# Kernel tuning notes

Hardware: AMD Instinct MI355X
Metric: run time of the kernel (lower is better)

Reference implementation:

```python
import jax, jax.numpy as jnp
import numpy as np

LR = 1.0
THRESHOLD = 0.5
EPS = 1e-8


def _hebbian_mask(x, H):
    # x: [B, x_size], H: [y_size, x_size]
    xn = x / jnp.linalg.norm(x, axis=1, keepdims=True)
    y = xn @ H.T                                   # [B, y_size]
    yn = y / jnp.linalg.norm(y, axis=1, keepdims=True)
    theta = jnp.mean(yn ** 2)                      # scalar
    # sum over batch of outer products == GEMM: [y_size, x_size]
    H_new = H + LR * (jnp.einsum('by,bx->yx', yn, xn) - theta * H)
    score = jnp.sum(H_new, axis=1)                 # [y_size]
    score = (score - jnp.min(score)) / (jnp.max(score) - jnp.min(score) + EPS)
    return jnp.where(score < THRESHOLD, 0.0, 1.0).astype(x.dtype)


def setup_inputs() -> dict:
    key = jax.random.key(0)
    ks = jax.random.split(key, 12)
    B, D_IN, D_OUT = 8192, 1024, 1000
    h = [256, 128, 64]
    inp = {
        'x': jax.random.normal(ks[0], (B, D_IN), dtype=jnp.float32),
        'mask0': jnp.ones((h[0],), dtype=jnp.float32),
        'mask1': jnp.ones((h[1],), dtype=jnp.float32),
        'mask2': jnp.ones((h[2],), dtype=jnp.float32),
        # linear layer params (torch Linear: y = x @ W.T + b)
        'W1': jax.random.normal(ks[1], (h[0], D_IN), dtype=jnp.float32) * 0.02,
        'b1': jnp.zeros((h[0],), dtype=jnp.float32),
        'W2': jax.random.normal(ks[2], (h[1], h[0]), dtype=jnp.float32) * 0.02,
        'b2': jnp.zeros((h[1],), dtype=jnp.float32),
        'W3': jax.random.normal(ks[3], (h[2], h[1]), dtype=jnp.float32) * 0.02,
        'b3': jnp.zeros((h[2],), dtype=jnp.float32),
        'W4': jax.random.normal(ks[4], (D_OUT, h[2]), dtype=jnp.float32) * 0.02,
        'b4': jnp.zeros((D_OUT,), dtype=jnp.float32),
        # hebbian params, init N(0, 0.01) as in the module (4th never used in forward)
        'H1': jax.random.normal(ks[5], (h[0], D_IN), dtype=jnp.float32) * 0.01,
        'H2': jax.random.normal(ks[6], (h[1], h[0]), dtype=jnp.float32) * 0.01,
        'H3': jax.random.normal(ks[7], (h[2], h[1]), dtype=jnp.float32) * 0.01,
    }
    return inp


def reference(x, mask0, mask1, mask2, W1, b1, W2, b2, W3, b3, W4, b4, H1, H2, H3):
    # layer 1 (hebbian uses the layer *input*)
    hm0 = _hebbian_mask(x, H1)
    x1 = jax.nn.relu(x @ W1.T + b1) * mask0
    # layer 2
    hm1 = _hebbian_mask(x1, H2)
    x2 = jax.nn.relu(x1 @ W2.T + b2) * mask1
    # layer 3
    hm2 = _hebbian_mask(x2, H3)
    x3 = jax.nn.relu(x2 @ W3.T + b3) * mask2
    # layer 4 (relu applied, no mask, no hebbian)
    out = jax.nn.relu(x3 @ W4.T + b4)
    return (out, hm0, hm1, hm2)
```

## Files before the change

kernel.cpp:

```cpp
#include <hip/hip_runtime.h>
#include <math.h>

typedef __attribute__((ext_vector_type(8))) short short8;
typedef __attribute__((ext_vector_type(4))) float floatx4;

typedef __attribute__((address_space(1))) const unsigned int as1_uint;
typedef __attribute__((address_space(3))) unsigned int as3_uint;
#define GLD16(g, l) __builtin_amdgcn_global_load_lds((as1_uint*)(g), (as3_uint*)(l), 16, 0, 0)

__device__ __forceinline__ unsigned short f2bf(float f) {
    unsigned int u = __float_as_uint(f);
    return (unsigned short)((u + 0x7fffu + ((u >> 16) & 1u)) >> 16);
}
__device__ __forceinline__ float bf2f(unsigned short h) {
    return __uint_as_float(((unsigned int)h) << 16);
}

__global__ __launch_bounds__(256) void convert_x(
    const float* __restrict__ x, unsigned short* __restrict__ Axhl,
    float* __restrict__ rs1, float* __restrict__ rq1,
    float* __restrict__ rs2, float* __restrict__ rq2,
    float* __restrict__ rs3, float* __restrict__ rq3,
    float* __restrict__ score, int* __restrict__ ctr)
{
    const int row = blockIdx.x, tid = threadIdx.x;
    if (row == 0) { score[tid] = 0.f; if (tid < 8) ctr[tid] = 0; }
    if (tid == 0) { rs2[row] = 0.f; rq2[row] = 0.f; rs3[row] = 0.f; rq3[row] = 0.f; }
    float4 v = *(const float4*)(x + (size_t)row * 1024 + (tid << 2));
    ushort4 h, l;
    h.x = f2bf(v.x); l.x = f2bf(v.x - bf2f(h.x));
    h.y = f2bf(v.y); l.y = f2bf(v.y - bf2f(h.y));
    h.z = f2bf(v.z); l.z = f2bf(v.z - bf2f(h.z));
    h.w = f2bf(v.w); l.w = f2bf(v.w - bf2f(h.w));
    *(ushort4*)(Axhl + (size_t)row * 2048 + (tid << 2)) = h;
    *(ushort4*)(Axhl + (size_t)row * 2048 + 1024 + (tid << 2)) = l;
    float s = v.x + v.y + v.z + v.w;
    float qq = v.x*v.x + v.y*v.y + v.z*v.z + v.w*v.w;
#pragma unroll
    for (int d = 1; d < 64; d <<= 1) { s += __shfl_xor(s, d, 64); qq += __shfl_xor(qq, d, 64); }
    __shared__ float sS[4], sQ[4];
    if ((tid & 63) == 0) { sS[tid >> 6] = s; sQ[tid >> 6] = qq; }
    __syncthreads();
    if (tid == 0) {
        rs1[row] = sS[0] + sS[1] + sS[2] + sS[3];
        rq1[row] = sQ[0] + sQ[1] + sQ[2] + sQ[3];
    }
}

__global__ __launch_bounds__(256) void convert_w(
    const float* __restrict__ H1, const float* __restrict__ W1,
    const float* __restrict__ H2, const float* __restrict__ W2,
    const float* __restrict__ H3, const float* __restrict__ W3,
    const float* __restrict__ W4,
    unsigned short* __restrict__ B1, unsigned short* __restrict__ B2,
    unsigned short* __restrict__ B3, unsigned short* __restrict__ B4,
    float* __restrict__ rsH1, float* __restrict__ rsH2, float* __restrict__ rsH3)
{
    const int b = blockIdx.x, tid = threadIdx.x;
    const float* src; unsigned short* dst; int K; float* rsum = nullptr;
    if (b < 256)      { K = 1024; src = H1 + (size_t)b * 1024;        dst = B1 + (size_t)b * 2048;        rsum = rsH1 + b; }
    else if (b < 512) { K = 1024; src = W1 + (size_t)(b - 256) * 1024; dst = B1 + (size_t)b * 2048; }
    else if (b < 640) { K = 256;  src = H2 + (size_t)(b - 512) * 256;  dst = B2 + (size_t)(b - 512) * 512; rsum = rsH2 + (b - 512); }
    else if (b < 768) { K = 256;  src = W2 + (size_t)(b - 640) * 256;  dst = B2 + (size_t)(b - 512) * 512; }
    else if (b < 832) { K = 128;  src = H3 + (size_t)(b - 768) * 128;  dst = B3 + (size_t)(b - 768) * 256; rsum = rsH3 + (b - 768); }
    else if (b < 896) { K = 128;  src = W3 + (size_t)(b - 832) * 128;  dst = B3 + (size_t)(b - 768) * 256; }
    else { K = 64; int r = b - 896; src = (r < 1000) ? (W4 + (size_t)r * 64) : nullptr; dst = B4 + (size_t)r * 128; }

    float lsum = 0.f;
    if (tid * 4 < K) {
        float4 v = src ? *(const float4*)(src + tid * 4) : make_float4(0.f, 0.f, 0.f, 0.f);
        ushort4 h, l;
        h.x = f2bf(v.x); l.x = f2bf(v.x - bf2f(h.x));
        h.y = f2bf(v.y); l.y = f2bf(v.y - bf2f(h.y));
        h.z = f2bf(v.z); l.z = f2bf(v.z - bf2f(h.z));
        h.w = f2bf(v.w); l.w = f2bf(v.w - bf2f(h.w));
        *(ushort4*)(dst + tid * 4) = h;
        *(ushort4*)(dst + K + tid * 4) = l;
        lsum = v.x + v.y + v.z + v.w;
    }
    if (rsum) {
#pragma unroll
        for (int d = 1; d < 64; d <<= 1) lsum += __shfl_xor(lsum, d, 64);
        __shared__ float sS[4];
        if ((tid & 63) == 0) sS[tid >> 6] = lsum;
        __syncthreads();
        if (tid == 0) *rsum = sS[0] + sS[1] + sS[2] + sS[3];
    }
}

#define KW 64
__global__ __launch_bounds__(256) void mfma_layer(
    const unsigned short* __restrict__ Ag, const unsigned short* __restrict__ Bg,
    const float* __restrict__ bias, const float* __restrict__ maskv,
    float* __restrict__ T, unsigned short* __restrict__ Xhl,
    float* __restrict__ outF,
    float* __restrict__ rs, float* __restrict__ rq,
    int K, int Nh, int Nw, int NwReal)
{
    constexpr int CPR = 8;
    constexpr int PERW = 4;
    constexpr int TILEB = 128 * 128;
    __shared__ __align__(16) char lds[4 * TILEB];

    const int tid = threadIdx.x;
    const int w = tid >> 6, lane = tid & 63;
    const int q = lane >> 4, m16 = lane & 15;
    const int wm = w & 1, wn = w >> 1;

    const int lin = blockIdx.y * gridDim.x + blockIdx.x;
    const int g = lin & 7, s = lin >> 3;
    const int by = g + ((s & 7) << 3);
    const int bx = s >> 3;

    const int strideB = 4 * K;
    const int u = lane & 7, v = lane >> 3;
    int aOff[PERW], bOff[PERW];
#pragma unroll
    for (int t0 = 0; t0 < PERW; ++t0) {
        const int t = w * PERW + t0;
        const int r = t * 8 + v;
        const int c = u ^ (r & 7);
        aOff[t0] = (by * 128 + r) * strideB + c * 16;
        bOff[t0] = (bx * 128 + r) * strideB + c * 16;
    }

    const char* Ab = (const char*)Ag;
    const char* Bb = (const char*)Bg;
    floatx4 acc[4][4] = {};

    const int kiters = K / KW;
    const int NIT = 3 * kiters;

    auto stage = [&](int buf, int it) {
        const int seg = it / kiters;
        const int k0 = (it - seg * kiters) * KW;
        const int ka = ((seg == 1) ? 2 * K : 0) + 2 * k0;
        const int kb = ((seg == 2) ? 2 * K : 0) + 2 * k0;
        char* base = lds + buf * 2 * TILEB;
#pragma unroll
        for (int t0 = 0; t0 < PERW; ++t0) {
            const int t = w * PERW + t0;
            GLD16(Ab + aOff[t0] + ka, base + t * 1024);
            GLD16(Bb + bOff[t0] + kb, base + TILEB + t * 1024);
        }
    };

    stage(0, 0);
    int cur = 0;
    for (int it = 0; it < NIT; ++it) {
        __syncthreads();
        if (it + 1 < NIT) stage(cur ^ 1, it + 1);
        const char* pb = lds + cur * 2 * TILEB;
#pragma unroll
        for (int h = 0; h < 2; ++h) {
            short8 af[4], bfr[4];
#pragma unroll
            for (int i = 0; i < 4; ++i) {
                const int ra = wm * 64 + i * 16 + m16;
                af[i] = *(const short8*)(pb + ra * 128 + (((h * 4 + q) ^ (ra & 7)) << 4));
                const int rb = wn * 64 + i * 16 + m16;
                bfr[i] = *(const short8*)(pb + TILEB + rb * 128 + (((h * 4 + q) ^ (rb & 7)) << 4));
            }
#pragma unroll
            for (int i = 0; i < 4; ++i)
#pragma unroll
                for (int j = 0; j < 4; ++j)
                    acc[i][j] = __builtin_amdgcn_mfma_f32_16x16x32_bf16(af[i], bfr[j], acc[i][j], 0, 0, 0);
        }
        cur ^= 1;
    }

    const int colW = bx * 128 + wn * 64;
    const bool isHwave = (outF == nullptr) && (colW < Nh);
#pragma unroll
    for (int i = 0; i < 4; ++i) {
        const int row0 = by * 128 + wm * 64 + i * 16 + q * 4;
        float rsum[4] = {0.f, 0.f, 0.f, 0.f}, rqsum[4] = {0.f, 0.f, 0.f, 0.f};
#pragma unroll
        for (int j = 0; j < 4; ++j) {
            const int col = colW + j * 16 + m16;
            floatx4 vv = acc[i][j];
            if (outF) {
                if (col < NwReal) {
                    const float bb = bias[col];
#pragma unroll
                    for (int rg = 0; rg < 4; ++rg)
                        outF[(size_t)(row0 + rg) * NwReal + col] = fmaxf(vv[rg] + bb, 0.f);
                }
            } else if (isHwave) {
#pragma unroll
                for (int rg = 0; rg < 4; ++rg)
                    T[(size_t)(row0 + rg) * Nh + col] = vv[rg];
            } else {
                const int c = col - Nh;
                const float bb = bias[c], mm = maskv[c];
#pragma unroll
                for (int rg = 0; rg < 4; ++rg) {
                    const float xv = fmaxf(vv[rg] + bb, 0.f) * mm;
                    const unsigned short hi = f2bf(xv);
                    const unsigned short lo = f2bf(xv - bf2f(hi));
                    Xhl[(size_t)(row0 + rg) * (2 * Nw) + c] = hi;
                    Xhl[(size_t)(row0 + rg) * (2 * Nw) + Nw + c] = lo;
                    rsum[rg] += xv; rqsum[rg] += xv * xv;
                }
            }
        }
        if (rs && !isHwave && !outF) {
#pragma unroll
            for (int rg = 0; rg < 4; ++rg) {
                float a_ = rsum[rg], b_ = rqsum[rg];
#pragma unroll
                for (int d = 1; d < 16; d <<= 1) {
                    a_ += __shfl_xor(a_, d, 64);
                    b_ += __shfl_xor(b_, d, 64);
                }
                if (m16 == 0) {
                    atomicAdd(&rs[row0 + rg], a_);
                    atomicAdd(&rq[row0 + rg], b_);
                }
            }
        }
    }
}

__global__ __launch_bounds__(256) void hebb_finish(
    const float* __restrict__ T, const float* __restrict__ rs,
    const float* __restrict__ rq, const float* __restrict__ rowsumH,
    float* __restrict__ score, int* __restrict__ counter,
    float* __restrict__ hm, int ysize)
{
    const int tid = threadIdx.x, lane = tid & 63, wave = tid >> 6;
    const int vecsz = ysize >> 6;
    const int b0 = blockIdx.x * 64;
    float accv[4] = {0.f, 0.f, 0.f, 0.f};
    for (int r = wave; r < 64; r += 4) {
        const float* Trow = T + (size_t)(b0 + r) * ysize;
        float vals[4] = {0.f, 0.f, 0.f, 0.f};
        if (vecsz == 4) { float4 t = *(const float4*)(Trow + (lane << 2)); vals[0]=t.x; vals[1]=t.y; vals[2]=t.z; vals[3]=t.w; }
        else if (vecsz == 2) { float2 t = *(const float2*)(Trow + (lane << 1)); vals[0]=t.x; vals[1]=t.y; }
        else vals[0] = Trow[lane];
        float sq = vals[0]*vals[0] + vals[1]*vals[1] + vals[2]*vals[2] + vals[3]*vals[3];
#pragma unroll
        for (int i = 1; i < 64; i <<= 1) sq += __shfl_xor(sq, i, 64);
        const float wgt = rs[b0 + r] / (sqrtf(rq[b0 + r]) * sqrtf(sq));
        for (int j = 0; j < 4; ++j) accv[j] += vals[j] * wgt;
    }
    __shared__ float sPart[4][256];
    for (int j = 0; j < vecsz; ++j) sPart[wave][lane * vecsz + j] = accv[j];
    __syncthreads();
    if (tid < ysize)
        atomicAdd(&score[tid], sPart[0][tid] + sPart[1][tid] + sPart[2][tid] + sPart[3][tid]);
    __syncthreads();
    __shared__ int lastFlag;
    if (tid == 0) {
        __threadfence();
        lastFlag = (atomicAdd(counter, 1) == (int)gridDim.x - 1) ? 1 : 0;
    }
    __syncthreads();
    if (!lastFlag) return;
    float full = 0.f;
    if (tid < ysize) {
        float sc = atomicAdd(&score[tid], 0.f);
        full = (1.f - 1.f / (float)ysize) * rowsumH[tid] + sc;
    }
    __shared__ float sMin[256], sMax[256];
    sMin[tid] = (tid < ysize) ? full : 3.4e38f;
    sMax[tid] = (tid < ysize) ? full : -3.4e38f;
    __syncthreads();
    for (int st = 128; st > 0; st >>= 1) {
        if (tid < st) { sMin[tid] = fminf(sMin[tid], sMin[tid+st]); sMax[tid] = fmaxf(sMax[tid], sMax[tid+st]); }
        __syncthreads();
    }
    if (tid < ysize) {
        float nrm = (full - sMin[0]) / (sMax[0] - sMin[0] + 1e-8f);
        hm[tid] = (nrm < 0.5f) ? 0.f : 1.f;
    }
    score[tid] = 0.f;
}

extern "C" void kernel_launch(void* const* d_in, const int* in_sizes, int n_in,
                              void* d_out, int out_size, void* d_ws, size_t ws_size,
                              hipStream_t stream)
{
    const float* x     = (const float*)d_in[0];
    const float* mask0 = (const float*)d_in[1];
    const float* mask1 = (const float*)d_in[2];
    const float* mask2 = (const float*)d_in[3];
    const float* W1 = (const float*)d_in[4];  const float* b1 = (const float*)d_in[5];
    const float* W2 = (const float*)d_in[6];  const float* b2 = (const float*)d_in[7];
    const float* W3 = (const float*)d_in[8];  const float* b3 = (const float*)d_in[9];
    const float* W4 = (const float*)d_in[10]; const float* b4 = (const float*)d_in[11];
    const float* H1 = (const float*)d_in[12];
    const float* H2 = (const float*)d_in[13];
    const float* H3 = (const float*)d_in[14];

    float* out = (float*)d_out;
    float* hm0 = out + (size_t)8192 * 1000;
    float* hm1 = hm0 + 256;
    float* hm2 = hm1 + 128;

    float* ws = (float*)d_ws;
    unsigned short* Axhl = (unsigned short*)ws;
    unsigned short* X2hl = (unsigned short*)ws;
    unsigned short* X3hl = (unsigned short*)(ws + 1048576);
    float* p = ws + 8388608;
    unsigned short* B1 = (unsigned short*)p;  p += 524288;
    unsigned short* B2 = (unsigned short*)p;  p += 65536;
    unsigned short* B3 = (unsigned short*)p;  p += 16384;
    unsigned short* B4 = (unsigned short*)p;  p += 65536;
    float* T    = p;  p += 2097152;
    unsigned short* X1hl = (unsigned short*)p; p += 2097152;
    float* rs1 = p; p += 8192;  float* rq1 = p; p += 8192;
    float* rs2 = p; p += 8192;  float* rq2 = p; p += 8192;
    float* rs3 = p; p += 8192;  float* rq3 = p; p += 8192;
    float* rsH1 = p; p += 256;  float* rsH2 = p; p += 128;  float* rsH3 = p; p += 64;
    float* score = p; p += 256;
    int* ctr = (int*)p;

    convert_x<<<8192, 256, 0, stream>>>(x, Axhl, rs1, rq1, rs2, rq2, rs3, rq3, score, ctr);
    convert_w<<<1920, 256, 0, stream>>>(H1, W1, H2, W2, H3, W3, W4, B1, B2, B3, B4, rsH1, rsH2, rsH3);

    mfma_layer<<<dim3(4, 64), 256, 0, stream>>>(
        Axhl, B1, b1, mask0, T, X1hl, nullptr, rs2, rq2, 1024, 256, 256, 256);
    hebb_finish<<<128, 256, 0, stream>>>(T, rs1, rq1, rsH1, score, ctr + 0, hm0, 256);

    mfma_layer<<<dim3(2, 64), 256, 0, stream>>>(
        X1hl, B2, b2, mask1, T, X2hl, nullptr, rs3, rq3, 256, 128, 128, 128);
    hebb_finish<<<128, 256, 0, stream>>>(T, rs2, rq2, rsH2, score, ctr + 1, hm1, 128);

    mfma_layer<<<dim3(1, 64), 256, 0, stream>>>(
        X2hl, B3, b3, mask2, T, X3hl, nullptr, nullptr, nullptr, 128, 64, 64, 64);
    hebb_finish<<<128, 256, 0, stream>>>(T, rs3, rq3, rsH3, score, ctr + 2, hm2, 64);

    mfma_layer<<<dim3(8, 64), 256, 0, stream>>>(
        X3hl, B4, b4, nullptr, nullptr, nullptr, out, nullptr, nullptr, 64, 0, 1024, 1000);
}
```

Baseline: 243.5 us.

## Template MFMA layer on tile size and fuse split-bf16 passes per k-step

The GEMM kernel is templated on the M/N tile (128x64 or 64x64), so layers with small N launch more blocks and fill more CUs. The hi/lo bf16 split products (hh, lh, hl) are now computed together within each 32-wide k-step instead of in three sequential passes over K. Both the hi and lo parts of A and B are staged into LDS per step. The block-to-tile mapping is generalized for any grid height. Smaller tiles lower per-block data reuse and raise global traffic relative to compute.

```diff
diff --git a/kernel.cpp b/kernel.cpp
--- a/kernel.cpp
+++ b/kernel.cpp
@@ -88,7 +88,7 @@
     }
 }
 
-#define KW 64
+template<int TM, int TN>
 __global__ __launch_bounds__(256) void mfma_layer(
     const unsigned short* __restrict__ Ag, const unsigned short* __restrict__ Bg,
     const float* __restrict__ bias, const float* __restrict__ maskv,
@@ -97,10 +97,14 @@
     float* __restrict__ rs, float* __restrict__ rq,
     int K, int Nh, int Nw, int NwReal)
 {
-    constexpr int CPR = 8;
-    constexpr int PERW = 4;
-    constexpr int TILEB = 128 * 128;
-    __shared__ __align__(16) char lds[4 * TILEB];
+    constexpr int MI = TM / 32;
+    constexpr int NJ = TN / 32;
+    constexpr int IA = TM / 16;
+    constexpr int IB = TN / 16;
+    constexpr int NI = 2 * (IA + IB);
+    constexpr int PERW = NI / 4;
+    constexpr int BUFB = NI * 1024;
+    __shared__ __align__(16) char lds[2 * BUFB];
 
     const int tid = threadIdx.x;
     const int w = tid >> 6, lane = tid & 63;
@@ -108,76 +112,77 @@
     const int wm = w & 1, wn = w >> 1;
 
     const int lin = blockIdx.y * gridDim.x + blockIdx.x;
-    const int g = lin & 7, s = lin >> 3;
-    const int by = g + ((s & 7) << 3);
-    const int bx = s >> 3;
+    const int g = lin & 7, idx = lin >> 3;
+    const int rows8 = gridDim.y >> 3;
+    const int by = g + 8 * (idx % rows8);
+    const int bx = idx / rows8;
 
     const int strideB = 4 * K;
-    const int u = lane & 7, v = lane >> 3;
-    int aOff[PERW], bOff[PERW];
+    const int v = lane >> 2, u = lane & 3;
+
+    const char* srcp[PERW];
 #pragma unroll
     for (int t0 = 0; t0 < PERW; ++t0) {
         const int t = w * PERW + t0;
-        const int r = t * 8 + v;
-        const int c = u ^ (r & 7);
-        aOff[t0] = (by * 128 + r) * strideB + c * 16;
-        bOff[t0] = (bx * 128 + r) * strideB + c * 16;
-    }
-
-    const char* Ab = (const char*)Ag;
-    const char* Bb = (const char*)Bg;
-    floatx4 acc[4][4] = {};
-
-    const int kiters = K / KW;
-    const int NIT = 3 * kiters;
-
-    auto stage = [&](int buf, int it) {
-        const int seg = it / kiters;
-        const int k0 = (it - seg * kiters) * KW;
-        const int ka = ((seg == 1) ? 2 * K : 0) + 2 * k0;
-        const int kb = ((seg == 2) ? 2 * K : 0) + 2 * k0;
-        char* base = lds + buf * 2 * TILEB;
-#pragma unroll
-        for (int t0 = 0; t0 < PERW; ++t0) {
-            const int t = w * PERW + t0;
-            GLD16(Ab + aOff[t0] + ka, base + t * 1024);
-            GLD16(Bb + bOff[t0] + kb, base + TILEB + t * 1024);
-        }
+        int rloc; const char* base;
+        if (t < IA)               { rloc = t * 16 + v;                base = (const char*)Ag + (size_t)(by * TM + rloc) * strideB; }
+        else if (t < 2 * IA)      { rloc = (t - IA) * 16 + v;         base = (const char*)Ag + (size_t)(by * TM + rloc) * strideB + 2 * K; }
+        else if (t < 2 * IA + IB) { rloc = (t - 2 * IA) * 16 + v;     base = (const char*)Bg + (size_t)(bx * TN + rloc) * strideB; }
+        else                      { rloc = (t - 2 * IA - IB) * 16 + v; base = (const char*)Bg + (size_t)(bx * TN + rloc) * strideB + 2 * K; }
+        srcp[t0] = base + ((u ^ (rloc & 3)) << 4);
+    }
+
+    auto stage = [&](int buf, int k0) {
+        char* dst = lds + buf * BUFB + (w * PERW) * 1024;
+        const int kb = 2 * k0;
+#pragma unroll
+        for (int t0 = 0; t0 < PERW; ++t0)
+            GLD16(srcp[t0] + kb, dst + t0 * 1024);
     };
+
+    floatx4 acc[MI][NJ] = {};
+    const int NIT = K / 32;
 
     stage(0, 0);
     int cur = 0;
     for (int it = 0; it < NIT; ++it) {
         __syncthreads();
-        if (it + 1 < NIT) stage(cur ^ 1, it + 1);
-        const char* pb = lds + cur * 2 * TILEB;
-#pragma unroll
-        for (int h = 0; h < 2; ++h) {
-            short8 af[4], bfr[4];
-#pragma unroll
-            for (int i = 0; i < 4; ++i) {
-                const int ra = wm * 64 + i * 16 + m16;
-                af[i] = *(const short8*)(pb + ra * 128 + (((h * 4 + q) ^ (ra & 7)) << 4));
-                const int rb = wn * 64 + i * 16 + m16;
-                bfr[i] = *(const short8*)(pb + TILEB + rb * 128 + (((h * 4 + q) ^ (rb & 7)) << 4));
+        if (it + 1 < NIT) stage(cur ^ 1, (it + 1) * 32);
+        const char* pb = lds + cur * BUFB;
+        short8 ah[MI], al[MI], bh[NJ], bl[NJ];
+#pragma unroll
+        for (int i = 0; i < MI; ++i) {
+            const int ra = wm * (TM / 2) + i * 16 + m16;
+            const int so = (q ^ (ra & 3)) << 4;
+            ah[i] = *(const short8*)(pb + ra * 64 + so);
+            al[i] = *(const short8*)(pb + IA * 1024 + ra * 64 + so);
+        }
+#pragma unroll
+        for (int j = 0; j < NJ; ++j) {
+            const int rb = wn * (TN / 2) + j * 16 + m16;
+            const int so = (q ^ (rb & 3)) << 4;
+            bh[j] = *(const short8*)(pb + 2 * IA * 1024 + rb * 64 + so);
+            bl[j] = *(const short8*)(pb + (2 * IA + IB) * 1024 + rb * 64 + so);
+        }
+#pragma unroll
+        for (int i = 0; i < MI; ++i)
+#pragma unroll
+            for (int j = 0; j < NJ; ++j) {
+                acc[i][j] = __builtin_amdgcn_mfma_f32_16x16x32_bf16(ah[i], bh[j], acc[i][j], 0, 0, 0);
+                acc[i][j] = __builtin_amdgcn_mfma_f32_16x16x32_bf16(al[i], bh[j], acc[i][j], 0, 0, 0);
+                acc[i][j] = __builtin_amdgcn_mfma_f32_16x16x32_bf16(ah[i], bl[j], acc[i][j], 0, 0, 0);
             }
-#pragma unroll
-            for (int i = 0; i < 4; ++i)
-#pragma unroll
-                for (int j = 0; j < 4; ++j)
-                    acc[i][j] = __builtin_amdgcn_mfma_f32_16x16x32_bf16(af[i], bfr[j], acc[i][j], 0, 0, 0);
-        }
         cur ^= 1;
     }
 
-    const int colW = bx * 128 + wn * 64;
+    const int colW = bx * TN + wn * (TN / 2);
     const bool isHwave = (outF == nullptr) && (colW < Nh);
 #pragma unroll
-    for (int i = 0; i < 4; ++i) {
-        const int row0 = by * 128 + wm * 64 + i * 16 + q * 4;
+    for (int i = 0; i < MI; ++i) {
+        const int row0 = by * TM + wm * (TM / 2) + i * 16 + q * 4;
         float rsum[4] = {0.f, 0.f, 0.f, 0.f}, rqsum[4] = {0.f, 0.f, 0.f, 0.f};
 #pragma unroll
-        for (int j = 0; j < 4; ++j) {
+        for (int j = 0; j < NJ; ++j) {
             const int col = colW + j * 16 + m16;
             floatx4 vv = acc[i][j];
             if (outF) {
@@ -320,18 +325,18 @@
     convert_x<<<8192, 256, 0, stream>>>(x, Axhl, rs1, rq1, rs2, rq2, rs3, rq3, score, ctr);
     convert_w<<<1920, 256, 0, stream>>>(H1, W1, H2, W2, H3, W3, W4, B1, B2, B3, B4, rsH1, rsH2, rsH3);
 
-    mfma_layer<<<dim3(4, 64), 256, 0, stream>>>(
+    mfma_layer<128, 64><<<dim3(8, 64), 256, 0, stream>>>(
         Axhl, B1, b1, mask0, T, X1hl, nullptr, rs2, rq2, 1024, 256, 256, 256);
     hebb_finish<<<128, 256, 0, stream>>>(T, rs1, rq1, rsH1, score, ctr + 0, hm0, 256);
 
-    mfma_layer<<<dim3(2, 64), 256, 0, stream>>>(
+    mfma_layer<64, 64><<<dim3(4, 128), 256, 0, stream>>>(
         X1hl, B2, b2, mask1, T, X2hl, nullptr, rs3, rq3, 256, 128, 128, 128);
     hebb_finish<<<128, 256, 0, stream>>>(T, rs2, rq2, rsH2, score, ctr + 1, hm1, 128);
 
-    mfma_layer<<<dim3(1, 64), 256, 0, stream>>>(
+    mfma_layer<64, 64><<<dim3(2, 128), 256, 0, stream>>>(
         X2hl, B3, b3, mask2, T, X3hl, nullptr, nullptr, nullptr, 128, 64, 64, 64);
     hebb_finish<<<128, 256, 0, stream>>>(T, rs3, rq3, rsH3, score, ctr + 2, hm2, 64);
 
-    mfma_layer<<<dim3(8, 64), 256, 0, stream>>>(
+    mfma_layer<128, 64><<<dim3(16, 64), 256, 0, stream>>>(
         X3hl, B4, b4, nullptr, nullptr, nullptr, out, nullptr, nullptr, 64, 0, 1024, 1000);
 }
```

After: 225.8 us. 7.3% less time.
